# Kernel optimization log

Hardware: AMD Instinct MI355X
Metric: run time of the kernel (lower is better)

The kernel has to match this reference:

```python
import jax, jax.numpy as jnp
import numpy as np

EPS = 1e-8

def setup_inputs() -> dict:
    key = jax.random.key(0)
    ks = jax.random.split(key, 4)
    B, N, D, H = 8, 4096, 768, 256
    x = jax.random.normal(ks[0], (B, N, D), dtype=jnp.float32)
    W_base = jnp.ones((N, D), dtype=jnp.float32)
    modrelu_bias = jnp.full((D,), -0.1, dtype=jnp.float32)
    mlp_w1 = jax.random.normal(ks[1], (D, H), dtype=jnp.float32) * (1.0 / np.sqrt(D))
    mlp_b1 = jnp.zeros((H,), dtype=jnp.float32)
    mlp_w2 = jax.random.normal(ks[2], (H, D), dtype=jnp.float32) * (1.0 / np.sqrt(H))
    mlp_b2 = jnp.zeros((D,), dtype=jnp.float32)
    return {"x": x, "W_base": W_base, "modrelu_bias": modrelu_bias,
            "mlp_w1": mlp_w1, "mlp_b1": mlp_b1, "mlp_w2": mlp_w2, "mlp_b2": mlp_b2}

def reference(x, W_base, modrelu_bias, mlp_w1, mlp_b1, mlp_w2, mlp_b2):
    # FFT along last axis (embed_dim), matching tf.signal.fft semantics
    F = jnp.fft.fft(x.astype(jnp.complex64), axis=-1)  # (B, N, D) complex64
    # global context and adaptive filter delta
    c = jnp.mean(x, axis=1)                              # (B, D)
    h = jax.nn.gelu(c @ mlp_w1 + mlp_b1)                 # (B, H)
    delta_W = h @ mlp_w2 + mlp_b2                        # (B, D)
    W = W_base[None, :, :] + delta_W[:, None, :]         # (B, N, D)
    F_filtered = F * W.astype(jnp.complex64)
    # modReLU
    mag = jnp.abs(F_filtered)
    mag_act = jax.nn.relu(mag + modrelu_bias)
    scale = mag_act / jnp.maximum(mag, EPS)
    F_activated = F_filtered * scale.astype(jnp.complex64)
    Y = jnp.real(jnp.fft.ifft(F_activated, axis=-1)).astype(jnp.float32)
    return Y
```

## Files before the change

kernel.cpp:

```cpp
#include <hip/hip_runtime.h>
#include <math.h>

#define BDIM 8
#define NSEQ 4096
#define DDIM 768
#define HDIM 256
#define CH 64

__global__ __launch_bounds__(192)
void colsum_kernel(const float* __restrict__ x, float* __restrict__ csum) {
    int blk = blockIdx.x;
    int ch = blk % CH;
    int b  = blk / CH;
    int t  = threadIdx.x;
    const int nper = NSEQ / CH;
    const float4* p = reinterpret_cast<const float4*>(
        x + ((size_t)b * NSEQ + (size_t)ch * nper) * DDIM) + t;
    float4 acc = make_float4(0.f, 0.f, 0.f, 0.f);
    #pragma unroll 8
    for (int i = 0; i < nper; ++i) {
        float4 v = p[(size_t)i * (DDIM / 4)];
        acc.x += v.x; acc.y += v.y; acc.z += v.z; acc.w += v.w;
    }
    float* c = csum + b * DDIM + t * 4;
    atomicAdd(c + 0, acc.x);
    atomicAdd(c + 1, acc.y);
    atomicAdd(c + 2, acc.z);
    atomicAdd(c + 3, acc.w);
}

__global__ __launch_bounds__(256)
void dwinit_kernel(const float* __restrict__ b2, float* __restrict__ dW) {
    int idx = blockIdx.x * 256 + threadIdx.x;
    dW[idx] = b2[idx % DDIM];
}

__global__ __launch_bounds__(64)
void mlp_h_kernel(const float* __restrict__ csum, const float* __restrict__ w1,
                  const float* __restrict__ b1, float* __restrict__ h) {
    const int blk = blockIdx.x;
    const int hh = blk & (HDIM - 1);
    const int b  = blk >> 8;
    const int l  = threadIdx.x;
    const float* c = csum + b * DDIM;
    const float* w = w1 + hh;
    float acc = 0.f;
    #pragma unroll
    for (int j = 0; j < 12; ++j) {
        int d = l * 12 + j;
        acc = fmaf(c[d], w[(size_t)d * HDIM], acc);
    }
    #pragma unroll
    for (int off = 32; off; off >>= 1) acc += __shfl_down(acc, off);
    if (l == 0) {
        float a = acc * (1.0f / NSEQ) + b1[hh];
        float x3 = a * a * a;
        float g = 0.5f * a * (1.0f + tanhf(0.7978845608028654f * (a + 0.044715f * x3)));
        h[b * HDIM + hh] = g;
    }
}

__global__ __launch_bounds__(64)
void mlp_dw_kernel(const float* __restrict__ h, const float* __restrict__ w2,
                   float* __restrict__ dW) {
    const int blk = blockIdx.x;
    const int dc = blk % 12;
    const int jc = (blk / 12) & 3;
    const int b  = blk / 48;
    const int l  = threadIdx.x;
    __shared__ float hs[64];
    hs[l] = h[b * HDIM + jc * 64 + l];
    __syncthreads();
    const int d = dc * 64 + l;
    const float* w = w2 + (size_t)(jc * 64) * DDIM + d;
    float acc = 0.f;
    #pragma unroll 8
    for (int j = 0; j < 64; ++j) acc = fmaf(hs[j], w[(size_t)j * DDIM], acc);
    atomicAdd(&dW[b * DDIM + d], acc);
}


__device__ __forceinline__ void cmulc(float& r, float& i, float br, float bi) {
    float tr = r * br - i * bi;
    float ti = r * bi + i * br;
    r = tr; i = ti;
}

template<int M>
__device__ __forceinline__ float xsh(float v, int l) {
    int iv = __float_as_int(v);
    if constexpr (M == 1)       iv = __builtin_amdgcn_mov_dpp(iv, 0xB1, 0xF, 0xF, false);
    else if constexpr (M == 2)  iv = __builtin_amdgcn_mov_dpp(iv, 0x4E, 0xF, 0xF, false);
    else if constexpr (M == 32) iv = __builtin_amdgcn_ds_bpermute((l ^ 32) << 2, iv);
    else                        iv = __builtin_amdgcn_ds_swizzle(iv, (M << 10) | 0x1F);
    return __int_as_float(iv);
}

template<int M>
__device__ __forceinline__ void stage_fwd(float* zr, float* zi, int l) {
    float wc = 1.f, ws = 0.f;
    if constexpr (M > 1) {
        float jj = (float)(l & (M - 1));
        __sincosf(-(3.14159265358979323846f / M) * jj, &ws, &wc);
    }
    const bool hi = (l & M) != 0;
    const float sgn = hi ? -1.f : 1.f;
    #pragma unroll
    for (int j = 0; j < 12; ++j) {
        float pr = xsh<M>(zr[j], l), pi = xsh<M>(zi[j], l);
        float er = hi ? zr[j] : pr,  ei = hi ? zi[j] : pi;
        float o_r = hi ? pr : zr[j], o_i = hi ? pi : zi[j];
        float tr, ti;
        if constexpr (M > 1) { tr = wc * er - ws * ei; ti = wc * ei + ws * er; }
        else                 { tr = er; ti = ei; }
        zr[j] = fmaf(sgn, tr, o_r);
        zi[j] = fmaf(sgn, ti, o_i);
    }
}

template<int M>
__device__ __forceinline__ void stage_inv(float* zr, float* zi, int l) {
    float wc = 1.f, ws = 0.f;
    if constexpr (M > 1) {
        float jj = (float)(l & (M - 1));
        __sincosf((3.14159265358979323846f / M) * jj, &ws, &wc);
    }
    const bool hi = (l & M) != 0;
    const float sgn = hi ? -1.f : 1.f;
    const float wc2 = hi ? wc : 1.f;
    const float ws2 = hi ? ws : 0.f;
    #pragma unroll
    for (int j = 0; j < 12; ++j) {
        float pr = xsh<M>(zr[j], l), pi = xsh<M>(zi[j], l);
        float tr = fmaf(sgn, zr[j], pr);
        float ti = fmaf(sgn, zi[j], pi);
        zr[j] = wc2 * tr - ws2 * ti;
        zi[j] = wc2 * ti + ws2 * tr;
    }
}

template<bool INV>
__device__ __forceinline__ void dft12(float* zr, float* zi) {
    constexpr float C1 = 0.8660254037844386f;
    constexpr float SG = INV ? 1.f : -1.f;
    constexpr float E  = INV ? -C1 : C1;
    float sr[3][4], si[3][4];
    #pragma unroll
    for (int b = 0; b < 3; ++b) {
        float x0r = zr[b],     x0i = zi[b];
        float x1r = zr[3 + b], x1i = zi[3 + b];
        float x2r = zr[6 + b], x2i = zi[6 + b];
        float x3r = zr[9 + b], x3i = zi[9 + b];
        float t0r = x0r + x2r, t0i = x0i + x2i;
        float t1r = x0r - x2r, t1i = x0i - x2i;
        float t2r = x1r + x3r, t2i = x1i + x3i;
        float t3r = x1r - x3r, t3i = x1i - x3i;
        sr[b][0] = t0r + t2r; si[b][0] = t0i + t2i;
        sr[b][2] = t0r - t2r; si[b][2] = t0i - t2i;
        if constexpr (!INV) {
            sr[b][1] = t1r + t3i; si[b][1] = t1i - t3r;
            sr[b][3] = t1r - t3i; si[b][3] = t1i + t3r;
        } else {
            sr[b][1] = t1r - t3i; si[b][1] = t1i + t3r;
            sr[b][3] = t1r + t3i; si[b][3] = t1i - t3r;
        }
    }
    cmulc(sr[1][1], si[1][1], C1,  SG * 0.5f);
    cmulc(sr[1][2], si[1][2], 0.5f, SG * C1);
    { float t = sr[1][3]; sr[1][3] = -SG * si[1][3]; si[1][3] = SG * t; }
    cmulc(sr[2][1], si[2][1], 0.5f,  SG * C1);
    cmulc(sr[2][2], si[2][2], -0.5f, SG * C1);
    sr[2][3] = -sr[2][3]; si[2][3] = -si[2][3];
    #pragma unroll
    for (int p = 0; p < 4; ++p) {
        float x0r = sr[0][p], x0i = si[0][p];
        float x1r = sr[1][p], x1i = si[1][p];
        float x2r = sr[2][p], x2i = si[2][p];
        float tr = x1r + x2r, ti = x1i + x2i;
        float ur = x1r - x2r, ui = x1i - x2i;
        float br = x0r - 0.5f * tr, bi = x0i - 0.5f * ti;
        zr[p]     = x0r + tr;        zi[p]     = x0i + ti;
        zr[4 + p] = br + E * ui;     zi[4 + p] = bi - E * ur;
        zr[8 + p] = br - E * ui;     zi[8 + p] = bi + E * ur;
    }
}

__device__ __forceinline__ float geff2(float w, float m, float inv_m, float b) {
    float g = fmaf(__builtin_copysignf(1.0f, w), b * inv_m, w);
    return (fmaf(fabsf(w), m, b) > 0.0f) ? g : 0.0f;
}

__device__ __forceinline__ void filt_core(
    float Zkr, float Zki, float Znr, float Zni, int kx,
    const float* __restrict__ wb1, const float* __restrict__ wb2,
    const float* __restrict__ dwb, const float* __restrict__ bias,
    float& outR, float& outI) {
    const int nk = kx ? (DDIM - kx) : 0;
    float F1r = 0.5f * (Zkr + Znr), F1i = 0.5f * (Zki - Zni);
    float F2r = 0.5f * (Zki + Zni), F2i = 0.5f * (Znr - Zkr);
    float s1 = fmaxf(fmaf(F1r, F1r, F1i * F1i), 1e-24f);
    float s2 = fmaxf(fmaf(F2r, F2r, F2i * F2i), 1e-24f);
    float im1 = rsqrtf(s1), im2 = rsqrtf(s2);
    float m1 = s1 * im1,   m2 = s2 * im2;
    float dk = dwb[kx], dn = dwb[nk];
    float bk = bias[kx], bn = bias[nk];
    float w1k = wb1[kx] + dk, w1n = wb1[nk] + dn;
    float w2k = wb2[kx] + dk, w2n = wb2[nk] + dn;
    float g1 = 0.5f * (geff2(w1k, m1, im1, bk) + geff2(w1n, m1, im1, bn));
    float g2 = 0.5f * (geff2(w2k, m2, im2, bk) + geff2(w2n, m2, im2, bn));
    outR = g1 * F1r - g2 * F2i;
    outI = g1 * F1i + g2 * F2r;
}

template<int J>
__device__ __forceinline__ void filt_pair(
    float* zr, float* zi, float& svR, float& svI,
    int l, int src,
    const float* __restrict__ wb1, const float* __restrict__ wb2,
    const float* __restrict__ dwb, const float* __restrict__ bias) {
    constexpr int A = J, B = 11 - J;
    const float aZr = zr[A], aZi = zi[A];
    const float bZr = zr[B], bZi = zi[B];
    float paR = __int_as_float(__builtin_amdgcn_ds_bpermute(src, __float_as_int(bZr)));
    float paI = __int_as_float(__builtin_amdgcn_ds_bpermute(src, __float_as_int(bZi)));
    float pbR = __int_as_float(__builtin_amdgcn_ds_bpermute(src, __float_as_int(aZr)));
    float pbI = __int_as_float(__builtin_amdgcn_ds_bpermute(src, __float_as_int(aZi)));
    float a0r, a0i;
    if constexpr (J == 0) { a0r = aZr; a0i = aZi; }
    else                  { a0r = svR; a0i = svI; }
    float b0r, b0i;
    if constexpr (J == 5) { b0r = bZr; b0i = bZi; }
    else                  { b0r = zr[J + 1]; b0i = zi[J + 1]; }
    paR = (l == 0) ? a0r : paR;  paI = (l == 0) ? a0i : paI;
    pbR = (l == 0) ? b0r : pbR;  pbI = (l == 0) ? b0i : pbI;
    svR = bZr; svI = bZi;
    filt_core(aZr, aZi, paR, paI, 64 * A + l, wb1, wb2, dwb, bias, zr[A], zi[A]);
    filt_core(bZr, bZi, pbR, pbI, 64 * B + l, wb1, wb2, dwb, bias, zr[B], zi[B]);
}

__global__ __launch_bounds__(256, 4)
void fftmix_kernel(const float* __restrict__ x, const float* __restrict__ Wb,
                   const float* __restrict__ dW, const float* __restrict__ bias,
                   float* __restrict__ out) {
    const int l  = threadIdx.x & 63;
    const int wv = threadIdx.x >> 6;
    const int pair = blockIdx.x * 4 + wv;
    const int r1 = pair * 2;
    const int bb = r1 >> 12;
    const int sq = r1 & (NSEQ - 1);
    const int rl = __brev((unsigned)l) >> 26;

    float zr[12], zi[12];
    {
        const float4* p1 = reinterpret_cast<const float4*>(x + (size_t)r1 * DDIM + 12 * rl);
        const float4* p2 = reinterpret_cast<const float4*>(x + (size_t)(r1 + 1) * DDIM + 12 * rl);
        float4 a0 = p1[0], a1 = p1[1], a2 = p1[2];
        float4 b0 = p2[0], b1_ = p2[1], b2_ = p2[2];
        zr[0] = a0.x; zr[1] = a0.y; zr[2] = a0.z; zr[3] = a0.w;
        zr[4] = a1.x; zr[5] = a1.y; zr[6] = a1.z; zr[7] = a1.w;
        zr[8] = a2.x; zr[9] = a2.y; zr[10] = a2.z; zr[11] = a2.w;
        zi[0] = b0.x; zi[1] = b0.y; zi[2] = b0.z; zi[3] = b0.w;
        zi[4] = b1_.x; zi[5] = b1_.y; zi[6] = b1_.z; zi[7] = b1_.w;
        zi[8] = b2_.x; zi[9] = b2_.y; zi[10] = b2_.z; zi[11] = b2_.w;
    }

    stage_fwd<1>(zr, zi, l);  stage_fwd<2>(zr, zi, l);  stage_fwd<4>(zr, zi, l);
    stage_fwd<8>(zr, zi, l);  stage_fwd<16>(zr, zi, l); stage_fwd<32>(zr, zi, l);

    {
        const float th = -(6.283185307179586f / DDIM) * (float)l;
        #pragma unroll
        for (int j = 1; j < 12; ++j) {
            float s, c;
            __sincosf(th * (float)j, &s, &c);
            cmulc(zr[j], zi[j], c, s);
        }
    }

    dft12<false>(zr, zi);

    {
        const int src = ((64 - l) & 63) << 2;
        const float* wb1 = Wb + (size_t)sq * DDIM;
        const float* wb2 = wb1 + DDIM;
        const float* dwb = dW + (size_t)bb * DDIM;
        float svR = 0.f, svI = 0.f;
        filt_pair<0>(zr, zi, svR, svI, l, src, wb1, wb2, dwb, bias);
        filt_pair<1>(zr, zi, svR, svI, l, src, wb1, wb2, dwb, bias);
        filt_pair<2>(zr, zi, svR, svI, l, src, wb1, wb2, dwb, bias);
        filt_pair<3>(zr, zi, svR, svI, l, src, wb1, wb2, dwb, bias);
        filt_pair<4>(zr, zi, svR, svI, l, src, wb1, wb2, dwb, bias);
        filt_pair<5>(zr, zi, svR, svI, l, src, wb1, wb2, dwb, bias);
    }

    dft12<true>(zr, zi);

    {
        const float th = (6.283185307179586f / DDIM) * (float)l;
        #pragma unroll
        for (int j = 1; j < 12; ++j) {
            float s, c;
            __sincosf(th * (float)j, &s, &c);
            cmulc(zr[j], zi[j], c, s);
        }
    }

    stage_inv<32>(zr, zi, l); stage_inv<16>(zr, zi, l); stage_inv<8>(zr, zi, l);
    stage_inv<4>(zr, zi, l);  stage_inv<2>(zr, zi, l);  stage_inv<1>(zr, zi, l);

    {
        constexpr float inv = 1.0f / DDIM;
        float4* o1 = reinterpret_cast<float4*>(out + (size_t)r1 * DDIM + 12 * rl);
        float4* o2 = reinterpret_cast<float4*>(out + (size_t)(r1 + 1) * DDIM + 12 * rl);
        o1[0] = make_float4(zr[0] * inv, zr[1] * inv, zr[2] * inv, zr[3] * inv);
        o1[1] = make_float4(zr[4] * inv, zr[5] * inv, zr[6] * inv, zr[7] * inv);
        o1[2] = make_float4(zr[8] * inv, zr[9] * inv, zr[10] * inv, zr[11] * inv);
        o2[0] = make_float4(zi[0] * inv, zi[1] * inv, zi[2] * inv, zi[3] * inv);
        o2[1] = make_float4(zi[4] * inv, zi[5] * inv, zi[6] * inv, zi[7] * inv);
        o2[2] = make_float4(zi[8] * inv, zi[9] * inv, zi[10] * inv, zi[11] * inv);
    }
}

extern "C" void kernel_launch(void* const* d_in, const int* in_sizes, int n_in,
                              void* d_out, int out_size, void* d_ws, size_t ws_size,
                              hipStream_t stream) {
    const float* x    = (const float*)d_in[0];
    const float* Wb   = (const float*)d_in[1];
    const float* bias = (const float*)d_in[2];
    const float* w1   = (const float*)d_in[3];
    const float* b1   = (const float*)d_in[4];
    const float* w2   = (const float*)d_in[5];
    const float* b2   = (const float*)d_in[6];
    float* out = (float*)d_out;

    float* csum = (float*)d_ws;
    float* dW   = csum + BDIM * DDIM;
    float* h    = dW + BDIM * DDIM;

    hipMemsetAsync(csum, 0, BDIM * DDIM * sizeof(float), stream);
    dwinit_kernel<<<(BDIM * DDIM) / 256, 256, 0, stream>>>(b2, dW);
    colsum_kernel<<<BDIM * CH, 192, 0, stream>>>(x, csum);
    mlp_h_kernel<<<BDIM * HDIM, 64, 0, stream>>>(csum, w1, b1, h);
    mlp_dw_kernel<<<BDIM * 4 * 12, 64, 0, stream>>>(h, w2, dW);
    fftmix_kernel<<<(BDIM * NSEQ / 2) / 4, 256, 0, stream>>>(x, Wb, dW, bias, out);
}
```

Baseline: 118.4 us.

## Reorder FFT factorization to use coalesced strided loads and stores

Swaps the FFT decomposition order so the radix-12 step runs first on stride-64 elements and the cross-lane radix-2 stages run as decimation-in-frequency after it. This lets each lane load and store scalars at stride 64, so consecutive lanes touch consecutive addresses, instead of each lane reading bit-reversed 12-element float4 chunks. The filter stage now works in bit-reversed frequency order, with new lane-permutation indices for pairing k with D-k. The goal is better memory coalescing at the cost of scalar rather than vector memory instructions.

```diff
diff --git a/kernel.cpp b/kernel.cpp
--- a/kernel.cpp
+++ b/kernel.cpp
@@ -96,12 +96,13 @@
     return __int_as_float(iv);
 }
 
-template<int M>
-__device__ __forceinline__ void stage_fwd(float* zr, float* zi, int l) {
+template<int M, bool INV>
+__device__ __forceinline__ void stage_dit(float* zr, float* zi, int l) {
+    constexpr float SG = INV ? 1.f : -1.f;
     float wc = 1.f, ws = 0.f;
     if constexpr (M > 1) {
         float jj = (float)(l & (M - 1));
-        __sincosf(-(3.14159265358979323846f / M) * jj, &ws, &wc);
+        __sincosf(SG * (3.14159265358979323846f / M) * jj, &ws, &wc);
     }
     const bool hi = (l & M) != 0;
     const float sgn = hi ? -1.f : 1.f;
@@ -118,12 +119,13 @@
     }
 }
 
-template<int M>
-__device__ __forceinline__ void stage_inv(float* zr, float* zi, int l) {
+template<int M, bool INV>
+__device__ __forceinline__ void stage_dif(float* zr, float* zi, int l) {
+    constexpr float SG = INV ? 1.f : -1.f;
     float wc = 1.f, ws = 0.f;
     if constexpr (M > 1) {
         float jj = (float)(l & (M - 1));
-        __sincosf((3.14159265358979323846f / M) * jj, &ws, &wc);
+        __sincosf(SG * (3.14159265358979323846f / M) * jj, &ws, &wc);
     }
     const bool hi = (l & M) != 0;
     const float sgn = hi ? -1.f : 1.f;
@@ -212,30 +214,8 @@
     outI = g1 * F1i + g2 * F2r;
 }
 
-template<int J>
-__device__ __forceinline__ void filt_pair(
-    float* zr, float* zi, float& svR, float& svI,
-    int l, int src,
-    const float* __restrict__ wb1, const float* __restrict__ wb2,
-    const float* __restrict__ dwb, const float* __restrict__ bias) {
-    constexpr int A = J, B = 11 - J;
-    const float aZr = zr[A], aZi = zi[A];
-    const float bZr = zr[B], bZi = zi[B];
-    float paR = __int_as_float(__builtin_amdgcn_ds_bpermute(src, __float_as_int(bZr)));
-    float paI = __int_as_float(__builtin_amdgcn_ds_bpermute(src, __float_as_int(bZi)));
-    float pbR = __int_as_float(__builtin_amdgcn_ds_bpermute(src, __float_as_int(aZr)));
-    float pbI = __int_as_float(__builtin_amdgcn_ds_bpermute(src, __float_as_int(aZi)));
-    float a0r, a0i;
-    if constexpr (J == 0) { a0r = aZr; a0i = aZi; }
-    else                  { a0r = svR; a0i = svI; }
-    float b0r, b0i;
-    if constexpr (J == 5) { b0r = bZr; b0i = bZi; }
-    else                  { b0r = zr[J + 1]; b0i = zi[J + 1]; }
-    paR = (l == 0) ? a0r : paR;  paI = (l == 0) ? a0i : paI;
-    pbR = (l == 0) ? b0r : pbR;  pbI = (l == 0) ? b0i : pbI;
-    svR = bZr; svI = bZi;
-    filt_core(aZr, aZi, paR, paI, 64 * A + l, wb1, wb2, dwb, bias, zr[A], zi[A]);
-    filt_core(bZr, bZi, pbR, pbI, 64 * B + l, wb1, wb2, dwb, bias, zr[B], zi[B]);
+__device__ __forceinline__ float bperm(int src, float v) {
+    return __int_as_float(__builtin_amdgcn_ds_bpermute(src, __float_as_int(v)));
 }
 
 __global__ __launch_bounds__(256, 4)
@@ -248,24 +228,19 @@
     const int r1 = pair * 2;
     const int bb = r1 >> 12;
     const int sq = r1 & (NSEQ - 1);
-    const int rl = __brev((unsigned)l) >> 26;
 
     float zr[12], zi[12];
     {
-        const float4* p1 = reinterpret_cast<const float4*>(x + (size_t)r1 * DDIM + 12 * rl);
-        const float4* p2 = reinterpret_cast<const float4*>(x + (size_t)(r1 + 1) * DDIM + 12 * rl);
-        float4 a0 = p1[0], a1 = p1[1], a2 = p1[2];
-        float4 b0 = p2[0], b1_ = p2[1], b2_ = p2[2];
-        zr[0] = a0.x; zr[1] = a0.y; zr[2] = a0.z; zr[3] = a0.w;
-        zr[4] = a1.x; zr[5] = a1.y; zr[6] = a1.z; zr[7] = a1.w;
-        zr[8] = a2.x; zr[9] = a2.y; zr[10] = a2.z; zr[11] = a2.w;
-        zi[0] = b0.x; zi[1] = b0.y; zi[2] = b0.z; zi[3] = b0.w;
-        zi[4] = b1_.x; zi[5] = b1_.y; zi[6] = b1_.z; zi[7] = b1_.w;
-        zi[8] = b2_.x; zi[9] = b2_.y; zi[10] = b2_.z; zi[11] = b2_.w;
-    }
-
-    stage_fwd<1>(zr, zi, l);  stage_fwd<2>(zr, zi, l);  stage_fwd<4>(zr, zi, l);
-    stage_fwd<8>(zr, zi, l);  stage_fwd<16>(zr, zi, l); stage_fwd<32>(zr, zi, l);
+        const float* x1 = x + (size_t)r1 * DDIM + l;
+        const float* x2 = x1 + DDIM;
+        #pragma unroll
+        for (int j = 0; j < 12; ++j) {
+            zr[j] = x1[64 * j];
+            zi[j] = x2[64 * j];
+        }
+    }
+
+    dft12<false>(zr, zi);
 
     {
         const float th = -(6.283185307179586f / DDIM) * (float)l;
@@ -277,23 +252,42 @@
         }
     }
 
-    dft12<false>(zr, zi);
-
-    {
-        const int src = ((64 - l) & 63) << 2;
+    stage_dif<32, false>(zr, zi, l); stage_dif<16, false>(zr, zi, l);
+    stage_dif<8,  false>(zr, zi, l); stage_dif<4,  false>(zr, zi, l);
+    stage_dif<2,  false>(zr, zi, l); stage_dif<1,  false>(zr, zi, l);
+
+    {
+        const int rk = __brev((unsigned)l) >> 26;
+        const int src63 = (l ^ 63) << 2;
+        const int src0  = (__brev((unsigned)((64 - rk) & 63)) >> 26) << 2;
         const float* wb1 = Wb + (size_t)sq * DDIM;
         const float* wb2 = wb1 + DDIM;
         const float* dwb = dW + (size_t)bb * DDIM;
-        float svR = 0.f, svI = 0.f;
-        filt_pair<0>(zr, zi, svR, svI, l, src, wb1, wb2, dwb, bias);
-        filt_pair<1>(zr, zi, svR, svI, l, src, wb1, wb2, dwb, bias);
-        filt_pair<2>(zr, zi, svR, svI, l, src, wb1, wb2, dwb, bias);
-        filt_pair<3>(zr, zi, svR, svI, l, src, wb1, wb2, dwb, bias);
-        filt_pair<4>(zr, zi, svR, svI, l, src, wb1, wb2, dwb, bias);
-        filt_pair<5>(zr, zi, svR, svI, l, src, wb1, wb2, dwb, bias);
-    }
-
-    dft12<true>(zr, zi);
+        {
+            float a_r = zr[0], a_i = zi[0];
+            float p_r = bperm(src0, a_r), p_i = bperm(src0, a_i);
+            filt_core(a_r, a_i, p_r, p_i, 12 * rk, wb1, wb2, dwb, bias, zr[0], zi[0]);
+        }
+        {
+            float a_r = zr[6], a_i = zi[6];
+            float p_r = bperm(src63, a_r), p_i = bperm(src63, a_i);
+            filt_core(a_r, a_i, p_r, p_i, 6 + 12 * rk, wb1, wb2, dwb, bias, zr[6], zi[6]);
+        }
+        #pragma unroll
+        for (int a = 1; a <= 5; ++a) {
+            const int b = 12 - a;
+            float aR = zr[a], aI = zi[a];
+            float bR = zr[b], bI = zi[b];
+            float paR = bperm(src63, bR), paI = bperm(src63, bI);
+            float pbR = bperm(src63, aR), pbI = bperm(src63, aI);
+            filt_core(aR, aI, paR, paI, a + 12 * rk, wb1, wb2, dwb, bias, zr[a], zi[a]);
+            filt_core(bR, bI, pbR, pbI, b + 12 * rk, wb1, wb2, dwb, bias, zr[b], zi[b]);
+        }
+    }
+
+    stage_dit<1,  true>(zr, zi, l); stage_dit<2,  true>(zr, zi, l);
+    stage_dit<4,  true>(zr, zi, l); stage_dit<8,  true>(zr, zi, l);
+    stage_dit<16, true>(zr, zi, l); stage_dit<32, true>(zr, zi, l);
 
     {
         const float th = (6.283185307179586f / DDIM) * (float)l;
@@ -305,19 +299,17 @@
         }
     }
 
-    stage_inv<32>(zr, zi, l); stage_inv<16>(zr, zi, l); stage_inv<8>(zr, zi, l);
-    stage_inv<4>(zr, zi, l);  stage_inv<2>(zr, zi, l);  stage_inv<1>(zr, zi, l);
+    dft12<true>(zr, zi);
 
     {
         constexpr float inv = 1.0f / DDIM;
-        float4* o1 = reinterpret_cast<float4*>(out + (size_t)r1 * DDIM + 12 * rl);
-        float4* o2 = reinterpret_cast<float4*>(out + (size_t)(r1 + 1) * DDIM + 12 * rl);
-        o1[0] = make_float4(zr[0] * inv, zr[1] * inv, zr[2] * inv, zr[3] * inv);
-        o1[1] = make_float4(zr[4] * inv, zr[5] * inv, zr[6] * inv, zr[7] * inv);
-        o1[2] = make_float4(zr[8] * inv, zr[9] * inv, zr[10] * inv, zr[11] * inv);
-        o2[0] = make_float4(zi[0] * inv, zi[1] * inv, zi[2] * inv, zi[3] * inv);
-        o2[1] = make_float4(zi[4] * inv, zi[5] * inv, zi[6] * inv, zi[7] * inv);
-        o2[2] = make_float4(zi[8] * inv, zi[9] * inv, zi[10] * inv, zi[11] * inv);
+        float* o1 = out + (size_t)r1 * DDIM + l;
+        float* o2 = o1 + DDIM;
+        #pragma unroll
+        for (int j = 0; j < 12; ++j) {
+            o1[64 * j] = zr[j] * inv;
+            o2[64 * j] = zi[j] * inv;
+        }
     }
 }
 
```

New measurement: 149.5 us. 1.26x slower.

## Load and store FFT rows in natural lane order with bit-reversed processing indices

Applied to the files above, without the earlier changes.

Lanes now load and store contiguous 12-float chunks by lane id instead of bit-reversed lane id. The 64-point stages run as decimation-in-frequency forward and decimation-in-time inverse, with bit-reversed indices carried into the twiddles and the conjugate-partner permute. The goal is fully coalesced global loads and stores in the FFT mixing kernel. In exchange the stage ordering swaps, so the shuffle types used per stage (DPP, swizzle, bpermute) change, and the conjugate-pair lookup now needs an extra bit reversal.

```diff
diff --git a/kernel.cpp b/kernel.cpp
--- a/kernel.cpp
+++ b/kernel.cpp
@@ -86,52 +86,31 @@
     r = tr; i = ti;
 }
 
-template<int M>
+template<int MASK>
 __device__ __forceinline__ float xsh(float v, int l) {
     int iv = __float_as_int(v);
-    if constexpr (M == 1)       iv = __builtin_amdgcn_mov_dpp(iv, 0xB1, 0xF, 0xF, false);
-    else if constexpr (M == 2)  iv = __builtin_amdgcn_mov_dpp(iv, 0x4E, 0xF, 0xF, false);
-    else if constexpr (M == 32) iv = __builtin_amdgcn_ds_bpermute((l ^ 32) << 2, iv);
-    else                        iv = __builtin_amdgcn_ds_swizzle(iv, (M << 10) | 0x1F);
+    if constexpr (MASK == 1)       iv = __builtin_amdgcn_mov_dpp(iv, 0xB1, 0xF, 0xF, false);
+    else if constexpr (MASK == 2)  iv = __builtin_amdgcn_mov_dpp(iv, 0x4E, 0xF, 0xF, false);
+    else if constexpr (MASK == 32) iv = __builtin_amdgcn_ds_bpermute((l ^ 32) << 2, iv);
+    else                           iv = __builtin_amdgcn_ds_swizzle(iv, (MASK << 10) | 0x1F);
     return __int_as_float(iv);
 }
 
-template<int M>
-__device__ __forceinline__ void stage_fwd(float* zr, float* zi, int l) {
+template<int M, int MASK, bool INV>
+__device__ __forceinline__ void stageP(float* zr, float* zi, int l, int idx) {
+    constexpr float SG = INV ? 1.f : -1.f;
     float wc = 1.f, ws = 0.f;
     if constexpr (M > 1) {
-        float jj = (float)(l & (M - 1));
-        __sincosf(-(3.14159265358979323846f / M) * jj, &ws, &wc);
-    }
-    const bool hi = (l & M) != 0;
-    const float sgn = hi ? -1.f : 1.f;
-    #pragma unroll
-    for (int j = 0; j < 12; ++j) {
-        float pr = xsh<M>(zr[j], l), pi = xsh<M>(zi[j], l);
-        float er = hi ? zr[j] : pr,  ei = hi ? zi[j] : pi;
-        float o_r = hi ? pr : zr[j], o_i = hi ? pi : zi[j];
-        float tr, ti;
-        if constexpr (M > 1) { tr = wc * er - ws * ei; ti = wc * ei + ws * er; }
-        else                 { tr = er; ti = ei; }
-        zr[j] = fmaf(sgn, tr, o_r);
-        zi[j] = fmaf(sgn, ti, o_i);
-    }
-}
-
-template<int M>
-__device__ __forceinline__ void stage_inv(float* zr, float* zi, int l) {
-    float wc = 1.f, ws = 0.f;
-    if constexpr (M > 1) {
-        float jj = (float)(l & (M - 1));
-        __sincosf((3.14159265358979323846f / M) * jj, &ws, &wc);
-    }
-    const bool hi = (l & M) != 0;
+        float jj = (float)(idx & (M - 1));
+        __sincosf(SG * (3.14159265358979323846f / M) * jj, &ws, &wc);
+    }
+    const bool hi = (idx & M) != 0;
     const float sgn = hi ? -1.f : 1.f;
     const float wc2 = hi ? wc : 1.f;
     const float ws2 = hi ? ws : 0.f;
     #pragma unroll
     for (int j = 0; j < 12; ++j) {
-        float pr = xsh<M>(zr[j], l), pi = xsh<M>(zi[j], l);
+        float pr = xsh<MASK>(zr[j], l), pi = xsh<MASK>(zi[j], l);
         float tr = fmaf(sgn, zr[j], pr);
         float ti = fmaf(sgn, zi[j], pi);
         zr[j] = wc2 * tr - ws2 * ti;
@@ -215,7 +194,7 @@
 template<int J>
 __device__ __forceinline__ void filt_pair(
     float* zr, float* zi, float& svR, float& svI,
-    int l, int src,
+    int l, int rk, int src,
     const float* __restrict__ wb1, const float* __restrict__ wb2,
     const float* __restrict__ dwb, const float* __restrict__ bias) {
     constexpr int A = J, B = 11 - J;
@@ -234,8 +213,8 @@
     paR = (l == 0) ? a0r : paR;  paI = (l == 0) ? a0i : paI;
     pbR = (l == 0) ? b0r : pbR;  pbI = (l == 0) ? b0i : pbI;
     svR = bZr; svI = bZi;
-    filt_core(aZr, aZi, paR, paI, 64 * A + l, wb1, wb2, dwb, bias, zr[A], zi[A]);
-    filt_core(bZr, bZi, pbR, pbI, 64 * B + l, wb1, wb2, dwb, bias, zr[B], zi[B]);
+    filt_core(aZr, aZi, paR, paI, 64 * A + rk, wb1, wb2, dwb, bias, zr[A], zi[A]);
+    filt_core(bZr, bZi, pbR, pbI, 64 * B + rk, wb1, wb2, dwb, bias, zr[B], zi[B]);
 }
 
 __global__ __launch_bounds__(256, 4)
@@ -248,12 +227,12 @@
     const int r1 = pair * 2;
     const int bb = r1 >> 12;
     const int sq = r1 & (NSEQ - 1);
-    const int rl = __brev((unsigned)l) >> 26;
+    const int rk = __brev((unsigned)l) >> 26;
 
     float zr[12], zi[12];
     {
-        const float4* p1 = reinterpret_cast<const float4*>(x + (size_t)r1 * DDIM + 12 * rl);
-        const float4* p2 = reinterpret_cast<const float4*>(x + (size_t)(r1 + 1) * DDIM + 12 * rl);
+        const float4* p1 = reinterpret_cast<const float4*>(x + (size_t)r1 * DDIM + 12 * l);
+        const float4* p2 = reinterpret_cast<const float4*>(x + (size_t)(r1 + 1) * DDIM + 12 * l);
         float4 a0 = p1[0], a1 = p1[1], a2 = p1[2];
         float4 b0 = p2[0], b1_ = p2[1], b2_ = p2[2];
         zr[0] = a0.x; zr[1] = a0.y; zr[2] = a0.z; zr[3] = a0.w;
@@ -264,11 +243,12 @@
         zi[8] = b2_.x; zi[9] = b2_.y; zi[10] = b2_.z; zi[11] = b2_.w;
     }
 
-    stage_fwd<1>(zr, zi, l);  stage_fwd<2>(zr, zi, l);  stage_fwd<4>(zr, zi, l);
-    stage_fwd<8>(zr, zi, l);  stage_fwd<16>(zr, zi, l); stage_fwd<32>(zr, zi, l);
-
-    {
-        const float th = -(6.283185307179586f / DDIM) * (float)l;
+    stageP<32, 32, false>(zr, zi, l, l); stageP<16, 16, false>(zr, zi, l, l);
+    stageP<8,  8,  false>(zr, zi, l, l); stageP<4,  4,  false>(zr, zi, l, l);
+    stageP<2,  2,  false>(zr, zi, l, l); stageP<1,  1,  false>(zr, zi, l, l);
+
+    {
+        const float th = -(6.283185307179586f / DDIM) * (float)rk;
         #pragma unroll
         for (int j = 1; j < 12; ++j) {
             float s, c;
@@ -280,23 +260,24 @@
     dft12<false>(zr, zi);
 
     {
-        const int src = ((64 - l) & 63) << 2;
+        const int prk = (64 - rk) & 63;
+        const int src = ((__brev((unsigned)prk) >> 26)) << 2;
         const float* wb1 = Wb + (size_t)sq * DDIM;
         const float* wb2 = wb1 + DDIM;
         const float* dwb = dW + (size_t)bb * DDIM;
         float svR = 0.f, svI = 0.f;
-        filt_pair<0>(zr, zi, svR, svI, l, src, wb1, wb2, dwb, bias);
-        filt_pair<1>(zr, zi, svR, svI, l, src, wb1, wb2, dwb, bias);
-        filt_pair<2>(zr, zi, svR, svI, l, src, wb1, wb2, dwb, bias);
-        filt_pair<3>(zr, zi, svR, svI, l, src, wb1, wb2, dwb, bias);
-        filt_pair<4>(zr, zi, svR, svI, l, src, wb1, wb2, dwb, bias);
-        filt_pair<5>(zr, zi, svR, svI, l, src, wb1, wb2, dwb, bias);
+        filt_pair<0>(zr, zi, svR, svI, l, rk, src, wb1, wb2, dwb, bias);
+        filt_pair<1>(zr, zi, svR, svI, l, rk, src, wb1, wb2, dwb, bias);
+        filt_pair<2>(zr, zi, svR, svI, l, rk, src, wb1, wb2, dwb, bias);
+        filt_pair<3>(zr, zi, svR, svI, l, rk, src, wb1, wb2, dwb, bias);
+        filt_pair<4>(zr, zi, svR, svI, l, rk, src, wb1, wb2, dwb, bias);
+        filt_pair<5>(zr, zi, svR, svI, l, rk, src, wb1, wb2, dwb, bias);
     }
 
     dft12<true>(zr, zi);
 
     {
-        const float th = (6.283185307179586f / DDIM) * (float)l;
+        const float th = (6.283185307179586f / DDIM) * (float)rk;
         #pragma unroll
         for (int j = 1; j < 12; ++j) {
             float s, c;
@@ -305,13 +286,14 @@
         }
     }
 
-    stage_inv<32>(zr, zi, l); stage_inv<16>(zr, zi, l); stage_inv<8>(zr, zi, l);
-    stage_inv<4>(zr, zi, l);  stage_inv<2>(zr, zi, l);  stage_inv<1>(zr, zi, l);
+    stageP<32, 1,  true>(zr, zi, l, rk); stageP<16, 2,  true>(zr, zi, l, rk);
+    stageP<8,  4,  true>(zr, zi, l, rk); stageP<4,  8,  true>(zr, zi, l, rk);
+    stageP<2,  16, true>(zr, zi, l, rk); stageP<1,  32, true>(zr, zi, l, rk);
 
     {
         constexpr float inv = 1.0f / DDIM;
-        float4* o1 = reinterpret_cast<float4*>(out + (size_t)r1 * DDIM + 12 * rl);
-        float4* o2 = reinterpret_cast<float4*>(out + (size_t)(r1 + 1) * DDIM + 12 * rl);
+        float4* o1 = reinterpret_cast<float4*>(out + (size_t)r1 * DDIM + 12 * l);
+        float4* o2 = reinterpret_cast<float4*>(out + (size_t)(r1 + 1) * DDIM + 12 * l);
         o1[0] = make_float4(zr[0] * inv, zr[1] * inv, zr[2] * inv, zr[3] * inv);
         o1[1] = make_float4(zr[4] * inv, zr[5] * inv, zr[6] * inv, zr[7] * inv);
         o1[2] = make_float4(zr[8] * inv, zr[9] * inv, zr[10] * inv, zr[11] * inv);
```

Result: no change. 117.4 us (median of 2 runs) (-0.8%).
